# Kernel tuning notes

Hardware: AMD Instinct MI355X
Metric: run time of the kernel (lower is better)

Reference implementation:

```python
import jax, jax.numpy as jnp
import numpy as np

B, R, C, H, NB, NH, V = 1, 24, 128, 256, 2, 8, 32
DFF = 4 * H


def _ln(x, g, b):
    m = x.mean(-1, keepdims=True)
    v = x.var(-1, keepdims=True)
    return (x - m) / jnp.sqrt(v + 1e-5) * g + b


def _attn(x, wq, wk, wv, wo):
    # x: [..., S, H]; full (dense) multi-head self-attention over axis -2
    d = H // NH
    lead = x.shape[:-1]
    q = (x @ wq).reshape(*lead, NH, d)
    k = (x @ wk).reshape(*lead, NH, d)
    v = (x @ wv).reshape(*lead, NH, d)
    s = jnp.einsum('...qhd,...khd->...hqk', q, k) / np.float32(np.sqrt(d))
    p = jax.nn.softmax(s, axis=-1)
    o = jnp.einsum('...hqk,...khd->...qhd', p, v)
    return o.reshape(*lead, H) @ wo


def setup_inputs() -> dict:
    key = jax.random.key(0)
    ks = iter(jax.random.split(key, 40))

    def nrm(shape, s=0.02):
        return jax.random.normal(next(ks), shape, jnp.float32) * s

    # pair matrix: C(R,2) rows, each selecting (summing) two sequences
    pairs = np.array([(i, j) for i in range(R) for j in range(i + 1, R)], np.int64)
    P = pairs.shape[0]  # 276
    pm = np.zeros((P, R), np.float32)
    pm[np.arange(P)[:, None], pairs] = 1.0

    inp = {
        'x': jax.random.randint(next(ks), (B, R, C), 0, V, jnp.int32),
        'pm': jnp.asarray(pm),
        'emb': nrm((V, H), 1.0),
        'ln1_g': jnp.ones((NB, H)), 'ln1_b': jnp.zeros((NB, H)),
        'wq_r': nrm((NB, H, H)), 'wk_r': nrm((NB, H, H)),
        'wv_r': nrm((NB, H, H)), 'wo_r': nrm((NB, H, H)),
        'ln2_g': jnp.ones((NB, H)), 'ln2_b': jnp.zeros((NB, H)),
        'wq_c': nrm((NB, H, H)), 'wk_c': nrm((NB, H, H)),
        'wv_c': nrm((NB, H, H)), 'wo_c': nrm((NB, H, H)),
        'ln3_g': jnp.ones((NB, H)), 'ln3_b': jnp.zeros((NB, H)),
        'fw1': nrm((NB, H, DFF)), 'fb1': jnp.zeros((NB, DFF)),
        'fw2': nrm((NB, DFF, H)), 'fb2': jnp.zeros((NB, H)),
        'pw1': nrm((H, DFF)), 'pb1': jnp.zeros((DFF,)),
        'pw2': nrm((DFF, 1)), 'pb2': jnp.zeros((1,)),
        'uw': nrm((C, 1)), 'ub': jnp.zeros((1,)),
    }
    return inp


def reference(x, pm, emb, ln1_g, ln1_b, wq_r, wk_r, wv_r, wo_r,
              ln2_g, ln2_b, wq_c, wk_c, wv_c, wo_c, ln3_g, ln3_b,
              fw1, fb1, fw2, fb2, pw1, pb1, pw2, pb2, uw, ub):
    h = emb[x]                                   # [B,R,C,H]
    # pair_matrix @ x : pairwise gather-add over the row (sequence) axis
    h = jnp.einsum('pr,brch->bpch', pm, h)       # [B,P,C,H]
    for i in range(NB):
        # row attention: along columns C, independent per pair
        h = h + _attn(_ln(h, ln1_g[i], ln1_b[i]), wq_r[i], wk_r[i], wv_r[i], wo_r[i])
        # column attention: along pairs P, independent per column
        hc = jnp.swapaxes(h, 1, 2)               # [B,C,P,H]
        a = _attn(_ln(hc, ln2_g[i], ln2_b[i]), wq_c[i], wk_c[i], wv_c[i], wo_c[i])
        h = h + jnp.swapaxes(a, 1, 2)
        # feed-forward
        z = _ln(h, ln3_g[i], ln3_b[i])
        h = h + (jax.nn.gelu(z @ fw1[i] + fb1[i], approximate=False) @ fw2[i] + fb2[i])
    y = jax.nn.gelu(h @ pw1 + pb1, approximate=False) @ pw2 + pb2  # [B,P,C,1]
    y = y.squeeze(-1)                            # [B,P,C]
    y = (y @ uw + ub).squeeze(-1)                # [B,P]
    return y
```

## Files before the change

kernel.cpp:

```cpp
#include <hip/hip_runtime.h>
#include <math.h>

#define HH    256
#define NHEAD 8
#define HD    32
#define CC    128
#define RR    24
#define PP    276
#define NBLK  2
#define DFF   1024
#define MTOK  (PP*CC)

typedef float          f32x4  __attribute__((ext_vector_type(4)));
typedef short          bf16x8 __attribute__((ext_vector_type(8)));
typedef unsigned short u16;

__device__ __forceinline__ float gelu_f(float x) {
    return 0.5f * x * (1.0f + erff(x * 0.7071067811865476f));
}
__device__ __forceinline__ u16 f2b(float f) {
    unsigned u = __builtin_bit_cast(unsigned, f);
    unsigned r = (u + 0x7fffu + ((u >> 16) & 1u)) >> 16;
    return (u16)r;
}
__device__ __forceinline__ float b2f(u16 b) {
    unsigned u = ((unsigned)b) << 16;
    return __builtin_bit_cast(float, u);
}
__device__ __forceinline__ unsigned cvt_pk_bf16(float lo, float hi) {
    unsigned r;
    asm("v_cvt_pk_bf16_f32 %0, %1, %2" : "=v"(r) : "v"(lo), "v"(hi));
    return r;
}
__device__ __forceinline__ void gload16(const void* g, void* l) {
    __builtin_amdgcn_global_load_lds(
        (const __attribute__((address_space(1))) unsigned int*)g,
        (__attribute__((address_space(3))) unsigned int*)l, 16, 0, 0);
}

__global__ __launch_bounds__(256) void k_embed(
    const int* __restrict__ x, const float* __restrict__ pm,
    const float* __restrict__ emb, float* __restrict__ h) {
    const int p = blockIdx.x, c = blockIdx.y, t = threadIdx.x;
    float acc = 0.f;
    for (int r = 0; r < RR; ++r) {
        float w = pm[p * RR + r];
        if (w != 0.f) {
            int tok = x[r * CC + c];
            acc += w * emb[(size_t)tok * HH + t];
        }
    }
    h[((size_t)p * CC + c) * HH + t] = acc;
}

__global__ __launch_bounds__(256) void k_ln(
    const float* __restrict__ in, u16* __restrict__ out,
    const float* __restrict__ g, const float* __restrict__ b) {
    const int lane = threadIdx.x & 63, wid = threadIdx.x >> 6;
    const float4 gv = *(const float4*)&g[lane * 4];
    const float4 bv = *(const float4*)&b[lane * 4];
    #pragma unroll
    for (int rr = 0; rr < 2; ++rr) {
        const int row = blockIdx.x * 8 + wid * 2 + rr;
        const float4 v = *(const float4*)&in[(size_t)row * HH + lane * 4];
        float s  = v.x + v.y + v.z + v.w;
        float s2 = v.x * v.x + v.y * v.y + v.z * v.z + v.w * v.w;
        #pragma unroll
        for (int off = 32; off; off >>= 1) {
            s  += __shfl_xor(s,  off);
            s2 += __shfl_xor(s2, off);
        }
        const float mean = s * (1.f / HH);
        const float rstd = rsqrtf(s2 * (1.f / HH) - mean * mean + 1e-5f);
        const float o0 = (v.x - mean) * rstd * gv.x + bv.x;
        const float o1 = (v.y - mean) * rstd * gv.y + bv.y;
        const float o2 = (v.z - mean) * rstd * gv.z + bv.z;
        const float o3 = (v.w - mean) * rstd * gv.w + bv.w;
        uint2 o;
        o.x = cvt_pk_bf16(o0, o1);
        o.y = cvt_pk_bf16(o2, o3);
        *(uint2*)&out[(size_t)row * HH + lane * 4] = o;
    }
}

__global__ __launch_bounds__(256) void k_cvtT(
    const float* __restrict__ src, u16* __restrict__ dst,
    int R, int Cc, int dstStride, float mul) {
    __shared__ float tile[32][33];
    const size_t so = (size_t)blockIdx.z * R * Cc;
    const size_t dOff = (size_t)blockIdx.z * dstStride;
    const int r0 = blockIdx.x * 32, c0 = blockIdx.y * 32;
    const int tx = threadIdx.x & 31, ty = threadIdx.x >> 5;
    #pragma unroll
    for (int i = 0; i < 4; ++i)
        tile[ty + 8 * i][tx] = src[so + (size_t)(r0 + ty + 8 * i) * Cc + c0 + tx];
    __syncthreads();
    #pragma unroll
    for (int i = 0; i < 4; ++i)
        dst[dOff + (size_t)(c0 + ty + 8 * i) * R + r0 + tx] = f2b(mul * tile[tx][ty + 8 * i]);
}

#define BM 128
#define BN 64
#define BK 32
template<bool BIAS, bool GELU, bool RES, bool OF32, bool OBF16>
__global__ __launch_bounds__(256) void k_mgemm(
    const u16* __restrict__ A,
    const u16* __restrict__ Wt,
    const float* __restrict__ bias,
    float* __restrict__ C,
    u16* __restrict__ Cb,
    int M, int N, int K) {
    __shared__ __align__(16) u16 Al[3][BM * BK];
    __shared__ __align__(16) u16 Bl[3][BN * BK];
    const int tid = threadIdx.x;
    const int wid = tid >> 6, lane = tid & 63;
    const int wr = wid >> 1, wc = wid & 1;
    const int l16 = lane & 15, lh = lane >> 4;

    const int nwg = gridDim.x;
    const int ntx = N >> 6;
    const int swz = (blockIdx.x & 7) * (nwg >> 3) + (blockIdx.x >> 3);
    const int row0 = (swz / ntx) * BM, col0 = (swz % ntx) * BN;

    int rA[2], pA[2];
    #pragma unroll
    for (int i = 0; i < 2; ++i) {
        const int d = tid + i * 256;
        rA[i] = d >> 2;
        pA[i] = (d & 3) ^ ((rA[i] >> 1) & 3);
    }
    const int nB = tid >> 2;
    const int pB = (tid & 3) ^ ((nB >> 1) & 3);
    const int nt = K / BK;

    auto stage = [&](int buf, int kt) {
        #pragma unroll
        for (int i = 0; i < 2; ++i)
            gload16(A + (size_t)(row0 + rA[i]) * K + kt + pA[i] * 8,
                    (char*)&Al[buf][0] + (wid * 64 + i * 256) * 16);
        gload16(Wt + (size_t)(col0 + nB) * K + kt + pB * 8,
                (char*)&Bl[buf][0] + (wid * 64) * 16);
    };

    f32x4 acc[4][2];
    #pragma unroll
    for (int m = 0; m < 4; ++m)
        #pragma unroll
        for (int n = 0; n < 2; ++n) acc[m][n] = (f32x4){0.f, 0.f, 0.f, 0.f};

    stage(0, 0);
    stage(1, BK);
    for (int t = 0; t < nt; ++t) {
        const int cur = t % 3;
        if (t + 1 < nt) asm volatile("s_waitcnt vmcnt(3)" ::: "memory");
        else            asm volatile("s_waitcnt vmcnt(0)" ::: "memory");
        __builtin_amdgcn_s_barrier();
        __builtin_amdgcn_sched_barrier(0);
        if (t + 2 < nt) stage((t + 2) % 3, (t + 2) * BK);
        bf16x8 af[4], bfr[2];
        #pragma unroll
        for (int m = 0; m < 4; ++m) {
            const int r = wr * 64 + m * 16 + l16;
            af[m] = *(const bf16x8*)((const char*)&Al[cur][0]
                     + r * 64 + ((lh ^ ((r >> 1) & 3)) << 4));
        }
        #pragma unroll
        for (int n = 0; n < 2; ++n) {
            const int nn = wc * 32 + n * 16 + l16;
            bfr[n] = *(const bf16x8*)((const char*)&Bl[cur][0]
                     + nn * 64 + ((lh ^ ((nn >> 1) & 3)) << 4));
        }
        asm volatile("s_waitcnt lgkmcnt(0)" ::: "memory");
        __builtin_amdgcn_sched_barrier(0);
        __builtin_amdgcn_s_setprio(1);
        #pragma unroll
        for (int m = 0; m < 4; ++m)
            #pragma unroll
            for (int n = 0; n < 2; ++n)
                acc[m][n] = __builtin_amdgcn_mfma_f32_16x16x32_bf16(
                    bfr[n], af[m], acc[m][n], 0, 0, 0);
        __builtin_amdgcn_s_setprio(0);
    }
    const int lh4 = lh * 4;
    #pragma unroll
    for (int m = 0; m < 4; ++m) {
        const int rowg = row0 + wr * 64 + m * 16 + l16;
        #pragma unroll
        for (int n = 0; n < 2; ++n) {
            const int colg = col0 + wc * 32 + n * 16 + lh4;
            const size_t off = (size_t)rowg * N + colg;
            f32x4 v = acc[m][n];
            if (BIAS) v += *(const f32x4*)&bias[colg];
            if (GELU) {
                v[0] = gelu_f(v[0]); v[1] = gelu_f(v[1]);
                v[2] = gelu_f(v[2]); v[3] = gelu_f(v[3]);
            }
            if (RES) v += *(const f32x4*)&C[off];
            if (OF32) *(f32x4*)&C[off] = v;
            if (OBF16) {
                uint2 o;
                o.x = cvt_pk_bf16(v[0], v[1]);
                o.y = cvt_pk_bf16(v[2], v[3]);
                *(uint2*)&Cb[off] = o;
            }
        }
    }
}

template<int NQT>
__global__ __launch_bounds__(256) void k_fattn(
    const u16* __restrict__ qg, const u16* __restrict__ kg,
    const u16* __restrict__ vg, u16* __restrict__ og,
    int S, int base_mul, int stride, int rowH) {
    const int head = blockIdx.y;
    const int base = blockIdx.x * base_mul;
    const int tid  = threadIdx.x;
    const int w = tid >> 6, lane = tid & 63;
    const int l16 = lane & 15, lh = lane >> 4;

    __shared__ u16 Vt[32 * 296];

    const int nkt = (S + 15) >> 4;
    const int nch = (nkt + 1) >> 1;
    const int KP  = nch * 32;

    for (int it = tid; it < KP * 4; it += blockDim.x) {
        const int key = it >> 2, d8 = (it & 3) * 8;
        uint4 t4 = make_uint4(0u, 0u, 0u, 0u);
        if (key < S)
            t4 = *(const uint4*)(vg + (size_t)(base + key * stride) * rowH + head * HD + d8);
        Vt[(d8 + 0) * 296 + key] = (u16)(t4.x);
        Vt[(d8 + 1) * 296 + key] = (u16)(t4.x >> 16);
        Vt[(d8 + 2) * 296 + key] = (u16)(t4.y);
        Vt[(d8 + 3) * 296 + key] = (u16)(t4.y >> 16);
        Vt[(d8 + 4) * 296 + key] = (u16)(t4.z);
        Vt[(d8 + 5) * 296 + key] = (u16)(t4.z >> 16);
        Vt[(d8 + 6) * 296 + key] = (u16)(t4.w);
        Vt[(d8 + 7) * 296 + key] = (u16)(t4.w >> 16);
    }
    __syncthreads();

    bf16x8 qf[NQT];
    #pragma unroll
    for (int j = 0; j < NQT; ++j) {
        int qi = (w * NQT + j) * 16 + l16;
        int qc = qi < S ? qi : S - 1;
        qf[j] = *(const bf16x8*)(qg + (size_t)(base + qc * stride) * rowH + head * HD + lh * 8);
    }
    f32x4 acc[NQT][2];
    float mM[NQT], lL[NQT];
    #pragma unroll
    for (int j = 0; j < NQT; ++j) {
        acc[j][0] = (f32x4){0.f, 0.f, 0.f, 0.f};
        acc[j][1] = (f32x4){0.f, 0.f, 0.f, 0.f};
        mM[j] = -1e30f; lL[j] = 0.f;
    }

    auto ldK = [&](int kid) -> bf16x8 {
        int kc = kid < S ? kid : S - 1;
        return *(const bf16x8*)(kg + (size_t)(base + kc * stride) * rowH + head * HD + lh * 8);
    };
    auto ldV = [&](int ch, int dm) -> bf16x8 {
        return *(const bf16x8*)(Vt + (dm * 16 + l16) * 296 + ch * 32 + lh * 8);
    };

    bf16x8 kc0 = ldK(l16), kc1 = ldK(16 + l16);
    bf16x8 vc0 = ldV(0, 0), vc1 = ldV(0, 1);
    const int g0 = 2 * (lh & 1);
    const int src0 = l16 + 16 * g0, src1 = src0 + 16;
    const bool hiT = (lh >> 1) & 1;
    const int lh4 = lh * 4;

    for (int ch = 0; ch < nch; ++ch) {
        bf16x8 kn0, kn1, vn0, vn1;
        if (ch + 1 < nch) {
            kn0 = ldK((ch + 1) * 32 + l16);
            kn1 = ldK((ch + 1) * 32 + 16 + l16);
            vn0 = ldV(ch + 1, 0);
            vn1 = ldV(ch + 1, 1);
        }
        const int kb = ch * 32;
        const bool fullv = (kb + 32 <= S);
        #pragma unroll
        for (int j = 0; j < NQT; ++j) {
            f32x4 s0 = __builtin_amdgcn_mfma_f32_16x16x32_bf16(
                kc0, qf[j], (f32x4){0.f, 0.f, 0.f, 0.f}, 0, 0, 0);
            f32x4 s1 = __builtin_amdgcn_mfma_f32_16x16x32_bf16(
                kc1, qf[j], (f32x4){0.f, 0.f, 0.f, 0.f}, 0, 0, 0);
            if (!fullv) {
                #pragma unroll
                for (int i = 0; i < 4; ++i) {
                    s0[i] = (kb + lh4 + i      < S) ? s0[i] : -1e30f;
                    s1[i] = (kb + 16 + lh4 + i < S) ? s1[i] : -1e30f;
                }
            }
            float mx = fmaxf(fmaxf(fmaxf(s0[0], s0[1]), fmaxf(s0[2], s0[3])),
                             fmaxf(fmaxf(s1[0], s1[1]), fmaxf(s1[2], s1[3])));
            mx = fmaxf(mx, __shfl_xor(mx, 16));
            mx = fmaxf(mx, __shfl_xor(mx, 32));
            const float mn = fmaxf(mM[j], mx);
            const float corr = __expf(mM[j] - mn);
            mM[j] = mn;
            float p0[4], p1[4], ls = 0.f;
            #pragma unroll
            for (int i = 0; i < 4; ++i) {
                p0[i] = __expf(s0[i] - mn); ls += p0[i];
                p1[i] = __expf(s1[i] - mn); ls += p1[i];
            }
            lL[j] = lL[j] * corr + ls;
            acc[j][0] *= corr;
            acc[j][1] *= corr;
            const int w00 = (int)cvt_pk_bf16(p0[0], p0[1]);
            const int w01 = (int)cvt_pk_bf16(p0[2], p0[3]);
            const int w10 = (int)cvt_pk_bf16(p1[0], p1[1]);
            const int w11 = (int)cvt_pk_bf16(p1[2], p1[3]);
            uint4 W;
            { int a = __shfl(w00, src0), b = __shfl(w10, src0); W.x = (unsigned)(hiT ? b : a); }
            { int a = __shfl(w01, src0), b = __shfl(w11, src0); W.y = (unsigned)(hiT ? b : a); }
            { int a = __shfl(w00, src1), b = __shfl(w10, src1); W.z = (unsigned)(hiT ? b : a); }
            { int a = __shfl(w01, src1), b = __shfl(w11, src1); W.w = (unsigned)(hiT ? b : a); }
            const bf16x8 pw = __builtin_bit_cast(bf16x8, W);
            acc[j][0] = __builtin_amdgcn_mfma_f32_16x16x32_bf16(vc0, pw, acc[j][0], 0, 0, 0);
            acc[j][1] = __builtin_amdgcn_mfma_f32_16x16x32_bf16(vc1, pw, acc[j][1], 0, 0, 0);
        }
        kc0 = kn0; kc1 = kn1; vc0 = vn0; vc1 = vn1;
    }

    #pragma unroll
    for (int j = 0; j < NQT; ++j) {
        float lf = lL[j];
        lf += __shfl_xor(lf, 16);
        lf += __shfl_xor(lf, 32);
        const float inv = 1.f / lf;
        const int qi = (w * NQT + j) * 16 + l16;
        if (qi < S) {
            u16* dst = og + (size_t)(base + qi * stride) * HH + head * HD + lh4;
            #pragma unroll
            for (int dm = 0; dm < 2; ++dm) {
                uint2 o2;
                o2.x = cvt_pk_bf16(acc[j][dm][0] * inv, acc[j][dm][1] * inv);
                o2.y = cvt_pk_bf16(acc[j][dm][2] * inv, acc[j][dm][3] * inv);
                *(uint2*)(dst + dm * 16) = o2;
            }
        }
    }
}

__global__ __launch_bounds__(256) void k_head1(
    const u16* __restrict__ g, const float* __restrict__ pw2,
    const float* __restrict__ pb2, float* __restrict__ y) {
    const int tok = blockIdx.x, t = threadIdx.x;
    const ushort4 r4 = *(const ushort4*)&g[(size_t)tok * DFF + t * 4];
    const float4  w4 = *(const float4*)&pw2[t * 4];
    float s = b2f(r4.x) * w4.x + b2f(r4.y) * w4.y
            + b2f(r4.z) * w4.z + b2f(r4.w) * w4.w;
    #pragma unroll
    for (int off = 32; off; off >>= 1) s += __shfl_down(s, off);
    __shared__ float sm[4];
    if ((t & 63) == 0) sm[t >> 6] = s;
    __syncthreads();
    if (t == 0) y[tok] = sm[0] + sm[1] + sm[2] + sm[3] + pb2[0];
}

__global__ __launch_bounds__(128) void k_head2(
    const float* __restrict__ y, const float* __restrict__ uw,
    const float* __restrict__ ub, float* __restrict__ out) {
    const int p = blockIdx.x, t = threadIdx.x;
    float s = y[(size_t)p * CC + t] * uw[t];
    #pragma unroll
    for (int off = 32; off; off >>= 1) s += __shfl_down(s, off);
    __shared__ float sm[2];
    if ((t & 63) == 0) sm[t >> 6] = s;
    __syncthreads();
    if (t == 0) out[p] = sm[0] + sm[1] + ub[0];
}

extern "C" void kernel_launch(void* const* d_in, const int* in_sizes, int n_in,
                              void* d_out, int out_size, void* d_ws, size_t ws_size,
                              hipStream_t stream) {
    (void)in_sizes; (void)n_in; (void)out_size; (void)ws_size;
    const int*   x    = (const int*)  d_in[0];
    const float* pm   = (const float*)d_in[1];
    const float* emb  = (const float*)d_in[2];
    const float* ln1g = (const float*)d_in[3];
    const float* ln1b = (const float*)d_in[4];
    const float* wqr  = (const float*)d_in[5];
    const float* wkr  = (const float*)d_in[6];
    const float* wvr  = (const float*)d_in[7];
    const float* wor  = (const float*)d_in[8];
    const float* ln2g = (const float*)d_in[9];
    const float* ln2b = (const float*)d_in[10];
    const float* wqc  = (const float*)d_in[11];
    const float* wkc  = (const float*)d_in[12];
    const float* wvc  = (const float*)d_in[13];
    const float* woc  = (const float*)d_in[14];
    const float* ln3g = (const float*)d_in[15];
    const float* ln3b = (const float*)d_in[16];
    const float* fw1  = (const float*)d_in[17];
    const float* fb1  = (const float*)d_in[18];
    const float* fw2  = (const float*)d_in[19];
    const float* fb2  = (const float*)d_in[20];
    const float* pw1  = (const float*)d_in[21];
    const float* pb1  = (const float*)d_in[22];
    const float* pw2  = (const float*)d_in[23];
    const float* pb2  = (const float*)d_in[24];
    const float* uw   = (const float*)d_in[25];
    const float* ub   = (const float*)d_in[26];
    float* out = (float*)d_out;

    char* wsp = (char*)d_ws;
    float* h   = (float*)wsp;
    u16*   zb  = (u16*)(wsp + 36175872);
    u16*   hb  = zb + (size_t)MTOK * HH;
    u16*   wts = hb + (size_t)MTOK * HH;
    float* yb  = (float*)((char*)wts + 4718592);
    u16*   scratch = (u16*)((char*)yb + 141312);
    u16* qkvb = scratch;
    u16* bigb = scratch;

    u16* wqkvr_t = wts;
    u16* wqkvc_t = wqkvr_t + 2 * 768 * HH;
    u16* wor_t   = wqkvc_t + 2 * 768 * HH;
    u16* woc_t   = wor_t + 2 * HH * HH;
    u16* fw1t    = woc_t + 2 * HH * HH;
    u16* fw2t    = fw1t + 2 * HH * DFF;
    u16* pw1t    = fw2t + 2 * HH * DFF;

    const float qscale = 0.17677669529663687f;
    const int QKVS = 768 * HH;

    k_cvtT<<<dim3(8, 8, 2),  256, 0, stream>>>(wqr, wqkvr_t,            HH, HH, QKVS, qscale);
    k_cvtT<<<dim3(8, 8, 2),  256, 0, stream>>>(wkr, wqkvr_t + 256 * HH, HH, HH, QKVS, 1.f);
    k_cvtT<<<dim3(8, 8, 2),  256, 0, stream>>>(wvr, wqkvr_t + 512 * HH, HH, HH, QKVS, 1.f);
    k_cvtT<<<dim3(8, 8, 2),  256, 0, stream>>>(wqc, wqkvc_t,            HH, HH, QKVS, qscale);
    k_cvtT<<<dim3(8, 8, 2),  256, 0, stream>>>(wkc, wqkvc_t + 256 * HH, HH, HH, QKVS, 1.f);
    k_cvtT<<<dim3(8, 8, 2),  256, 0, stream>>>(wvc, wqkvc_t + 512 * HH, HH, HH, QKVS, 1.f);
    k_cvtT<<<dim3(8, 8, 2),  256, 0, stream>>>(wor, wor_t, HH, HH, HH * HH, 1.f);
    k_cvtT<<<dim3(8, 8, 2),  256, 0, stream>>>(woc, woc_t, HH, HH, HH * HH, 1.f);
    k_cvtT<<<dim3(8, 32, 2), 256, 0, stream>>>(fw1, fw1t, HH, DFF, HH * DFF, 1.f);
    k_cvtT<<<dim3(32, 8, 2), 256, 0, stream>>>(fw2, fw2t, DFF, HH, HH * DFF, 1.f);
    k_cvtT<<<dim3(8, 32, 1), 256, 0, stream>>>(pw1, pw1t, HH, DFF, 0, 1.f);

    const int gQKV = (MTOK / BM) * (768 / BN);
    const int gO   = (MTOK / BM) * (HH  / BN);
    const int gUp  = (MTOK / BM) * (DFF / BN);

    k_embed<<<dim3(PP, CC), 256, 0, stream>>>(x, pm, emb, h);

    for (int i = 0; i < NBLK; ++i) {
        k_ln<<<MTOK / 8, 256, 0, stream>>>(h, zb, ln1g + i * HH, ln1b + i * HH);
        k_mgemm<false,false,false,false,true><<<gQKV, 256, 0, stream>>>(
            zb, wqkvr_t + (size_t)i * QKVS, nullptr, nullptr, qkvb, MTOK, 768, HH);
        k_fattn<2><<<dim3(PP, NHEAD), 256, 0, stream>>>(
            qkvb, qkvb + 256, qkvb + 512, zb, CC, CC, 1, 768);
        k_mgemm<false,false,true,true,false><<<gO, 256, 0, stream>>>(
            zb, wor_t + (size_t)i * HH * HH, nullptr, h, nullptr, MTOK, HH, HH);
        k_ln<<<MTOK / 8, 256, 0, stream>>>(h, zb, ln2g + i * HH, ln2b + i * HH);
        k_mgemm<false,false,false,false,true><<<gQKV, 256, 0, stream>>>(
            zb, wqkvc_t + (size_t)i * QKVS, nullptr, nullptr, qkvb, MTOK, 768, HH);
        k_fattn<6><<<dim3(CC, NHEAD), 192, 0, stream>>>(
            qkvb, qkvb + 256, qkvb + 512, zb, PP, 1, CC, 768);
        k_mgemm<false,false,true,true,false><<<gO, 256, 0, stream>>>(
            zb, woc_t + (size_t)i * HH * HH, nullptr, h, nullptr, MTOK, HH, HH);
        k_ln<<<MTOK / 8, 256, 0, stream>>>(h, zb, ln3g + i * HH, ln3b + i * HH);
        k_mgemm<true,true,false,false,true><<<gUp, 256, 0, stream>>>(
            zb, fw1t + (size_t)i * HH * DFF, fb1 + i * DFF, nullptr, bigb, MTOK, DFF, HH);
        if (i == NBLK - 1)
            k_mgemm<true,false,true,true,true><<<gO, 256, 0, stream>>>(
                bigb, fw2t + (size_t)i * HH * DFF, fb2 + i * HH, h, hb, MTOK, HH, DFF);
        else
            k_mgemm<true,false,true,true,false><<<gO, 256, 0, stream>>>(
                bigb, fw2t + (size_t)i * HH * DFF, fb2 + i * HH, h, nullptr, MTOK, HH, DFF);
    }

    k_mgemm<true,true,false,false,true><<<gUp, 256, 0, stream>>>(
        hb, pw1t, pb1, nullptr, bigb, MTOK, DFF, HH);
    k_head1<<<MTOK, 256, 0, stream>>>(bigb, pw2, pb2, yb);
    k_head2<<<PP, 128, 0, stream>>>(yb, uw, ub, out);
}
```

Before: 777.3 us.

## Pack V transpose as 32-bit pairs and split column attention over more waves

The V-transpose staging into shared memory now handles two keys per thread iteration and writes packed 32-bit words, halving the number of LDS stores and avoiding 16-bit partial writes. The column-attention launch moves from 3 waves with 6 query tiles each to 6 waves with 3 query tiles each (384 threads), with launch bounds raised to match. The next-chunk prefetch becomes unconditional by clamping the chunk index, which removes a branch. Raising launch bounds to 384 applies to both template instances and can lower the register budget, which may cause spills in the row-attention kernel.

```diff
diff --git a/kernel.cpp b/kernel.cpp
--- a/kernel.cpp
+++ b/kernel.cpp
@@ -209,7 +209,7 @@
 }
 
 template<int NQT>
-__global__ __launch_bounds__(256) void k_fattn(
+__global__ __launch_bounds__(384) void k_fattn(
     const u16* __restrict__ qg, const u16* __restrict__ kg,
     const u16* __restrict__ vg, u16* __restrict__ og,
     int S, int base_mul, int stride, int rowH) {
@@ -225,19 +225,21 @@
     const int nch = (nkt + 1) >> 1;
     const int KP  = nch * 32;
 
-    for (int it = tid; it < KP * 4; it += blockDim.x) {
-        const int key = it >> 2, d8 = (it & 3) * 8;
-        uint4 t4 = make_uint4(0u, 0u, 0u, 0u);
-        if (key < S)
-            t4 = *(const uint4*)(vg + (size_t)(base + key * stride) * rowH + head * HD + d8);
-        Vt[(d8 + 0) * 296 + key] = (u16)(t4.x);
-        Vt[(d8 + 1) * 296 + key] = (u16)(t4.x >> 16);
-        Vt[(d8 + 2) * 296 + key] = (u16)(t4.y);
-        Vt[(d8 + 3) * 296 + key] = (u16)(t4.y >> 16);
-        Vt[(d8 + 4) * 296 + key] = (u16)(t4.z);
-        Vt[(d8 + 5) * 296 + key] = (u16)(t4.z >> 16);
-        Vt[(d8 + 6) * 296 + key] = (u16)(t4.w);
-        Vt[(d8 + 7) * 296 + key] = (u16)(t4.w >> 16);
+    unsigned* Vw = (unsigned*)Vt;
+    for (int it = tid; it < (KP >> 1) * 4; it += blockDim.x) {
+        const int kp = it >> 2, d8 = (it & 3) * 8;
+        const int k0 = kp * 2, k1 = k0 + 1;
+        uint4 a = make_uint4(0u, 0u, 0u, 0u), b = a;
+        if (k0 < S) a = *(const uint4*)(vg + (size_t)(base + k0 * stride) * rowH + head * HD + d8);
+        if (k1 < S) b = *(const uint4*)(vg + (size_t)(base + k1 * stride) * rowH + head * HD + d8);
+        Vw[(d8 + 0) * 148 + kp] = (a.x & 0xffffu) | (b.x << 16);
+        Vw[(d8 + 1) * 148 + kp] = (a.x >> 16)     | (b.x & 0xffff0000u);
+        Vw[(d8 + 2) * 148 + kp] = (a.y & 0xffffu) | (b.y << 16);
+        Vw[(d8 + 3) * 148 + kp] = (a.y >> 16)     | (b.y & 0xffff0000u);
+        Vw[(d8 + 4) * 148 + kp] = (a.z & 0xffffu) | (b.z << 16);
+        Vw[(d8 + 5) * 148 + kp] = (a.z >> 16)     | (b.z & 0xffff0000u);
+        Vw[(d8 + 6) * 148 + kp] = (a.w & 0xffffu) | (b.w << 16);
+        Vw[(d8 + 7) * 148 + kp] = (a.w >> 16)     | (b.w & 0xffff0000u);
     }
     __syncthreads();
 
@@ -273,13 +275,11 @@
     const int lh4 = lh * 4;
 
     for (int ch = 0; ch < nch; ++ch) {
-        bf16x8 kn0, kn1, vn0, vn1;
-        if (ch + 1 < nch) {
-            kn0 = ldK((ch + 1) * 32 + l16);
-            kn1 = ldK((ch + 1) * 32 + 16 + l16);
-            vn0 = ldV(ch + 1, 0);
-            vn1 = ldV(ch + 1, 1);
-        }
+        const int chn = (ch + 1 < nch) ? ch + 1 : ch;
+        bf16x8 kn0 = ldK(chn * 32 + l16);
+        bf16x8 kn1 = ldK(chn * 32 + 16 + l16);
+        bf16x8 vn0 = ldV(chn, 0);
+        bf16x8 vn1 = ldV(chn, 1);
         const int kb = ch * 32;
         const bool fullv = (kb + 32 <= S);
         #pragma unroll
@@ -459,7 +459,7 @@
         k_ln<<<MTOK / 8, 256, 0, stream>>>(h, zb, ln2g + i * HH, ln2b + i * HH);
         k_mgemm<false,false,false,false,true><<<gQKV, 256, 0, stream>>>(
             zb, wqkvc_t + (size_t)i * QKVS, nullptr, nullptr, qkvb, MTOK, 768, HH);
-        k_fattn<6><<<dim3(CC, NHEAD), 192, 0, stream>>>(
+        k_fattn<3><<<dim3(CC, NHEAD), 384, 0, stream>>>(
             qkvb, qkvb + 256, qkvb + 512, zb, PP, 1, CC, 768);
         k_mgemm<false,false,true,true,false><<<gO, 256, 0, stream>>>(
             zb, woc_t + (size_t)i * HH * HH, nullptr, h, nullptr, MTOK, HH, HH);
```

New measurement: 741.4 us. -4.6%, faster.
